# Performance work log

Measured on AMD Instinct MI355X. Metric: run time of the kernel, lower is better.

The kernel has to match this reference:

```python
import jax, jax.numpy as jnp
import numpy as np

N_NODES = 100000


def sage_conv(x, edge_index, W_l, b_l, W_r):
    # PyG SAGEConv (mean aggr): out = lin_l(mean_{j in N(i)} x_j) + lin_r(x_i)
    src, dst = edge_index[0], edge_index[1]
    msgs = x[src]                                  # [E, F] gather
    agg = jax.ops.segment_sum(msgs, dst, num_segments=N_NODES)  # [N, F]
    deg = jax.ops.segment_sum(jnp.ones_like(src, dtype=x.dtype), dst, num_segments=N_NODES)
    mean = agg / jnp.maximum(deg, 1.0)[:, None]
    return mean @ W_l.T + b_l + x @ W_r.T


def setup_inputs() -> dict:
    key = jax.random.key(0)
    ks = jax.random.split(key, 12)
    D_in, D_h, D_e = 128, 256, 64
    E = 1600000
    x = jax.random.normal(ks[0], (N_NODES, D_in), dtype=jnp.float32)
    edge_index = jax.random.randint(ks[1], (2, E), 0, N_NODES, dtype=jnp.int64)

    def lin(k, out_d, in_d):
        s = 1.0 / np.sqrt(in_d)
        return jax.random.uniform(k, (out_d, in_d), jnp.float32, -s, s)

    params = {
        'W_l1': lin(ks[2], D_h, D_in), 'b_l1': jnp.zeros((D_h,), jnp.float32),
        'W_r1': lin(ks[3], D_h, D_in),
        'W_l2': lin(ks[4], D_e, D_h), 'b_l2': jnp.zeros((D_e,), jnp.float32),
        'W_r2': lin(ks[5], D_e, D_h),
        'fc1_W': lin(ks[6], D_h, D_e), 'fc1_b': jnp.zeros((D_h,), jnp.float32),
        'fc2_W': lin(ks[7], D_in, D_h), 'fc2_b': jnp.zeros((D_in,), jnp.float32),
    }
    return {'x': x, 'edge_index': edge_index, **params}


def reference(x, edge_index, W_l1, b_l1, W_r1, W_l2, b_l2, W_r2, fc1_W, fc1_b, fc2_W, fc2_b):
    # Encoder: two SAGEConv layers on LineItem nodes
    h = jax.nn.relu(sage_conv(x, edge_index, W_l1, b_l1, W_r1))
    emb = sage_conv(h, edge_index, W_l2, b_l2, W_r2)
    # Decoder: 2-layer MLP
    hid = jax.nn.relu(emb @ fc1_W.T + fc1_b)
    recon = hid @ fc2_W.T + fc2_b
    return emb, recon
```

## Files before the change

kernel.cpp:

```cpp
#include <hip/hip_runtime.h>
#include <hip/hip_bf16.h>

#define N_NODES 100000
#define D_IN 128
#define D_H 256
#define D_E 64
#define MT 32
#define BSHIFT 9
#define NBUCK ((N_NODES + 511) >> BSHIFT)
#define CHUNK 8192
#define RCR_T 1024
#define RCR_ILP (CHUNK / RCR_T)

typedef __attribute__((ext_vector_type(8))) short short8;
typedef __attribute__((ext_vector_type(4))) float floatx4;

__device__ inline unsigned short f2bf(float f) {
    union { float f; unsigned u; } v; v.f = f;
    unsigned r = v.u + 0x7FFF + ((v.u >> 16) & 1);
    return (unsigned short)(r >> 16);
}
__device__ inline unsigned f2bf2(float a, float b) {
    return (unsigned)f2bf(a) | ((unsigned)f2bf(b) << 16);
}
__device__ inline float2 bf2f2(unsigned v) {
    union { unsigned u; float f; } lo, hi;
    lo.u = v << 16;
    hi.u = v & 0xffff0000u;
    return make_float2(lo.f, hi.f);
}

#define MFMA16(a, b, c) __builtin_amdgcn_mfma_f32_16x16x32_bf16((a), (b), (c), 0, 0, 0)

__global__ void convert_weights(const float* __restrict__ Wl1, const float* __restrict__ Wr1,
                                const float* __restrict__ Wl2, const float* __restrict__ Wr2,
                                const float* __restrict__ fc1W, const float* __restrict__ fc2W,
                                unsigned short* __restrict__ W1s, unsigned short* __restrict__ W2s,
                                unsigned short* __restrict__ F1s, unsigned short* __restrict__ F2s) {
    int idx = blockIdx.x * blockDim.x + threadIdx.x;
    if (idx < 65536) {
        int out = idx >> 8, k = idx & 255;
        float v = (k < 128) ? Wl1[out * 128 + k] : Wr1[out * 128 + (k - 128)];
        int ks = k >> 5, quad = (k >> 3) & 3, e = k & 7, col = out & 15;
        int g = (out >> 4) * 8 + ks;
        W1s[(g * 64 + quad * 16 + col) * 8 + e] = f2bf(v);
    } else if (idx < 98304) {
        int i = idx - 65536; int out = i >> 8, k = i & 255;
        float v = (out < 64) ? Wl2[out * 256 + k] : Wr2[(out - 64) * 256 + k];
        int ks = k >> 5, quad = (k >> 3) & 3, e = k & 7, col = out & 15;
        int g = (out >> 4) * 8 + ks;
        W2s[(g * 64 + quad * 16 + col) * 8 + e] = f2bf(v);
    } else if (idx < 114688) {
        int i = idx - 98304;
        int out = i >> 6, k = i & 63;
        float v = fc1W[i];
        int ks = k >> 5, quad = (k >> 3) & 3, e = k & 7, col = out & 15;
        int g = (out >> 4) * 2 + ks;
        F1s[(g * 64 + quad * 16 + col) * 8 + e] = f2bf(v);
    } else if (idx < 147456) {
        int i = idx - 114688;
        int out = i >> 8, k = i & 255;
        float v = fc2W[i];
        int ks = k >> 5, quad = (k >> 3) & 3, e = k & 7, col = out & 15;
        int g = (out >> 4) * 8 + ks;
        F2s[(g * 64 + quad * 16 + col) * 8 + e] = f2bf(v);
    }
}

__global__ void convert_x(const float4* __restrict__ x4, uint2* __restrict__ xbf2, int total4) {
    int idx = blockIdx.x * blockDim.x + threadIdx.x;
    if (idx >= total4) return;
    float4 v = x4[idx];
    uint2 o;
    o.x = f2bf2(v.x, v.y);
    o.y = f2bf2(v.z, v.w);
    xbf2[idx] = o;
}

__global__ __launch_bounds__(RCR_T) void bucket_hist(
        const int* __restrict__ dst, int* __restrict__ bucketCnt, int E) {
    __shared__ int hist[256];
    const int t = threadIdx.x;
    if (t < 256) hist[t] = 0;
    __syncthreads();
    const int e0 = blockIdx.x * CHUNK;
    if (e0 + CHUNK <= E) {
        int dv[RCR_ILP];
#pragma unroll
        for (int i = 0; i < RCR_ILP; i++) dv[i] = dst[e0 + t + i * RCR_T];
#pragma unroll
        for (int i = 0; i < RCR_ILP; i++) atomicAdd(&hist[dv[i] >> BSHIFT], 1);
    } else {
        for (int e = e0 + t; e < E; e += RCR_T)
            atomicAdd(&hist[dst[e] >> BSHIFT], 1);
    }
    __syncthreads();
    if (t < NBUCK && hist[t] > 0) atomicAdd(&bucketCnt[t * 16], hist[t]);
}

__global__ void bucket_scan(const int* __restrict__ bucketCnt,
                            int* __restrict__ bucketOffs) {
    __shared__ int s[256];
    int t = threadIdx.x;
    int v = (t < NBUCK) ? bucketCnt[t * 16] : 0;
    s[t] = v;
    __syncthreads();
    for (int off = 1; off < 256; off <<= 1) {
        int tv = (t >= off) ? s[t - off] : 0;
        __syncthreads();
        s[t] += tv;
        __syncthreads();
    }
    if (t < NBUCK) bucketOffs[t] = s[t] - v;
    if (t == NBUCK - 1) bucketOffs[NBUCK] = s[t];
}

__global__ __launch_bounds__(RCR_T) void radix_count_reserve(
        const int* __restrict__ src, const int* __restrict__ dst,
        const int* __restrict__ bucketOffs, int* __restrict__ gcur,
        unsigned* __restrict__ pairs, int E) {
    __shared__ int hist[256];
    __shared__ int sBase[256];
    __shared__ int sCur[256];
    const int t = threadIdx.x;
    if (t < 256) { hist[t] = 0; sCur[t] = 0; }
    __syncthreads();
    const int e0 = blockIdx.x * CHUNK;

    if (e0 + CHUNK <= E) {
        int dv[RCR_ILP], sv[RCR_ILP];
#pragma unroll
        for (int i = 0; i < RCR_ILP; i++) dv[i] = dst[e0 + t + i * RCR_T];
#pragma unroll
        for (int i = 0; i < RCR_ILP; i++) atomicAdd(&hist[dv[i] >> BSHIFT], 1);
        __syncthreads();
        if (t < NBUCK && hist[t] > 0)
            sBase[t] = bucketOffs[t] + atomicAdd(&gcur[t * 16], hist[t]);
        __syncthreads();
#pragma unroll
        for (int i = 0; i < RCR_ILP; i++) sv[i] = src[e0 + t + i * RCR_T];
#pragma unroll
        for (int i = 0; i < RCR_ILP; i++) {
            int d = dv[i];
            int b = d >> BSHIFT;
            int pos = sBase[b] + atomicAdd(&sCur[b], 1);
            pairs[pos] = (unsigned)sv[i] | ((unsigned)(d & 511) << 20);
        }
    } else {
        const int e1 = E;
        for (int e = e0 + t; e < e1; e += RCR_T)
            atomicAdd(&hist[dst[e] >> BSHIFT], 1);
        __syncthreads();
        if (t < NBUCK && hist[t] > 0)
            sBase[t] = bucketOffs[t] + atomicAdd(&gcur[t * 16], hist[t]);
        __syncthreads();
        for (int e = e0 + t; e < e1; e += RCR_T) {
            int d = dst[e];
            int b = d >> BSHIFT;
            int pos = sBase[b] + atomicAdd(&sCur[b], 1);
            pairs[pos] = (unsigned)src[e] | ((unsigned)(d & 511) << 20);
        }
    }
}

__global__ __launch_bounds__(512) void radix_scatter2(
        const unsigned* __restrict__ pairs, const int* __restrict__ bucketOffs,
        int* __restrict__ degI, int* __restrict__ offs,
        int* __restrict__ srcS) {
    __shared__ int sCnt[512];
    __shared__ int sOff[512];
    const int b = blockIdx.x;
    const int lo = b << BSHIFT;
    const int t = threadIdx.x;
    sCnt[t] = 0;
    __syncthreads();
    const int start = bucketOffs[b];
    const int end = bucketOffs[b + 1];
    for (int i = start + t; i < end; i += 512)
        atomicAdd(&sCnt[pairs[i] >> 20], 1);
    __syncthreads();
    int v = sCnt[t];
    sOff[t] = v;
    __syncthreads();
    for (int off = 1; off < 512; off <<= 1) {
        int tv = (t >= off) ? sOff[t - off] : 0;
        __syncthreads();
        sOff[t] += tv;
        __syncthreads();
    }
    int excl = sOff[t] - v;
    int node = lo + t;
    if (node < N_NODES) {
        degI[node] = v;
        offs[node] = start + excl;
    }
    __syncthreads();
    sCnt[t] = start + excl;
    __syncthreads();
    int i = start + t;
    for (; i + 3 * 512 < end; i += 4 * 512) {
        unsigned p0 = pairs[i];
        unsigned p1 = pairs[i + 512];
        unsigned p2 = pairs[i + 1024];
        unsigned p3 = pairs[i + 1536];
        int dl0 = (int)(p0 >> 20), dl1 = (int)(p1 >> 20);
        int dl2 = (int)(p2 >> 20), dl3 = (int)(p3 >> 20);
        int q0 = atomicAdd(&sCnt[dl0], 1);
        int q1 = atomicAdd(&sCnt[dl1], 1);
        int q2 = atomicAdd(&sCnt[dl2], 1);
        int q3 = atomicAdd(&sCnt[dl3], 1);
        srcS[q0] = (int)(p0 & 0xFFFFFu);
        srcS[q1] = (int)(p1 & 0xFFFFFu);
        srcS[q2] = (int)(p2 & 0xFFFFFu);
        srcS[q3] = (int)(p3 & 0xFFFFFu);
    }
    for (; i < end; i += 512) {
        unsigned p = pairs[i];
        int dl = (int)(p >> 20);
        int pos = atomicAdd(&sCnt[dl], 1);
        srcS[pos] = (int)(p & 0xFFFFFu);
    }
}

#define ACC8(v)                                                   \
    { float2 f_;                                                  \
      f_ = bf2f2((v).x); s0 += f_.x; s1 += f_.y;                  \
      f_ = bf2f2((v).y); s2 += f_.x; s3 += f_.y;                  \
      f_ = bf2f2((v).z); s4 += f_.x; s5 += f_.y;                  \
      f_ = bf2f2((v).w); s6 += f_.x; s7 += f_.y; }

__global__ __launch_bounds__(256) void gather_mean_bf(
        const uint4* __restrict__ xb4, const int* __restrict__ srcS,
        const int* __restrict__ offs, const int* __restrict__ degI,
        uint4* __restrict__ mean4) {
    const int wave = threadIdx.x >> 6, lane = threadIdx.x & 63;
    const int q = lane >> 4, l16 = lane & 15;
    const int n = (blockIdx.x * 4 + wave) * 4 + q;
    if (n >= N_NODES) return;
    const int start = offs[n], cnt = degI[n];
    const int* sp = srcS + start;
    float s0 = 0.f, s1 = 0.f, s2 = 0.f, s3 = 0.f;
    float s4 = 0.f, s5 = 0.f, s6 = 0.f, s7 = 0.f;
    int j = 0;
    for (; j + 8 <= cnt; j += 8) {
        int i0 = sp[j],     i1 = sp[j + 1], i2 = sp[j + 2], i3 = sp[j + 3];
        int i4 = sp[j + 4], i5 = sp[j + 5], i6 = sp[j + 6], i7 = sp[j + 7];
        uint4 v0 = xb4[i0 * 16 + l16];
        uint4 v1 = xb4[i1 * 16 + l16];
        uint4 v2 = xb4[i2 * 16 + l16];
        uint4 v3 = xb4[i3 * 16 + l16];
        uint4 v4 = xb4[i4 * 16 + l16];
        uint4 v5 = xb4[i5 * 16 + l16];
        uint4 v6 = xb4[i6 * 16 + l16];
        uint4 v7 = xb4[i7 * 16 + l16];
        ACC8(v0); ACC8(v1); ACC8(v2); ACC8(v3);
        ACC8(v4); ACC8(v5); ACC8(v6); ACC8(v7);
    }
    for (; j + 4 <= cnt; j += 4) {
        int i0 = sp[j], i1 = sp[j + 1], i2 = sp[j + 2], i3 = sp[j + 3];
        uint4 v0 = xb4[i0 * 16 + l16];
        uint4 v1 = xb4[i1 * 16 + l16];
        uint4 v2 = xb4[i2 * 16 + l16];
        uint4 v3 = xb4[i3 * 16 + l16];
        ACC8(v0); ACC8(v1); ACC8(v2); ACC8(v3);
    }
    for (; j < cnt; j++) {
        uint4 v = xb4[sp[j] * 16 + l16];
        ACC8(v);
    }
    float rd = 1.0f / fmaxf((float)cnt, 1.0f);
    uint4 o;
    o.x = f2bf2(s0 * rd, s1 * rd);
    o.y = f2bf2(s2 * rd, s3 * rd);
    o.z = f2bf2(s4 * rd, s5 * rd);
    o.w = f2bf2(s6 * rd, s7 * rd);
    mean4[n * 16 + l16] = o;
}

__global__ __launch_bounds__(256, 4) void layer1_mfma(
        const unsigned* __restrict__ xbfu, const unsigned* __restrict__ meanbf,
        const unsigned short* __restrict__ W1s, const float* __restrict__ bl1,
        const unsigned short* __restrict__ W2s,
        unsigned short* __restrict__ z2bf, float* __restrict__ embOut) {
    __shared__ unsigned short sA[MT][264];
    __shared__ unsigned short sH[MT][264];
    const int tid = threadIdx.x;
    const int node0 = blockIdx.x * MT;

    const uint4* mean4 = (const uint4*)meanbf;
    const uint4* x4    = (const uint4*)xbfu;
#pragma unroll
    for (int it = 0; it < 4; it++) {
        int c = tid + it * 256;
        int row = c >> 5, half = (c >> 4) & 1, ci = c & 15;
        uint4 v = half ? x4[(node0 + row) * 16 + ci]
                       : mean4[(node0 + row) * 16 + ci];
        *(uint4*)&sA[row][half * 128 + ci * 8] = v;
    }
    __syncthreads();

    const int wave = tid >> 6, lane = tid & 63;
    const int col = lane & 15, quad = lane >> 4;

    floatx4 acc[2][4];
    const floatx4 zero = {0.f, 0.f, 0.f, 0.f};
#pragma unroll
    for (int mt = 0; mt < 2; mt++)
#pragma unroll
        for (int nt = 0; nt < 4; nt++) acc[mt][nt] = zero;

    const short8* w1base = (const short8*)W1s + wave * 2048 + lane;
#pragma unroll
    for (int ks = 0; ks < 8; ks++) {
        short8 a0 = *(const short8*)&sA[col][ks * 32 + quad * 8];
        short8 a1 = *(const short8*)&sA[16 + col][ks * 32 + quad * 8];
#pragma unroll
        for (int nt = 0; nt < 4; nt++) {
            short8 b = w1base[(nt * 8 + ks) * 64];
            acc[0][nt] = MFMA16(a0, b, acc[0][nt]);
            acc[1][nt] = MFMA16(a1, b, acc[1][nt]);
        }
    }

#pragma unroll
    for (int nt = 0; nt < 4; nt++) {
        int out = (wave * 4 + nt) * 16 + col;
        float bias = bl1[out];
#pragma unroll
        for (int mt = 0; mt < 2; mt++)
#pragma unroll
            for (int r = 0; r < 4; r++)
                sH[mt * 16 + quad * 4 + r][out] = f2bf(fmaxf(acc[mt][nt][r] + bias, 0.f));
    }
    __syncthreads();

    floatx4 acc2[2][2];
#pragma unroll
    for (int mt = 0; mt < 2; mt++)
#pragma unroll
        for (int nt = 0; nt < 2; nt++) acc2[mt][nt] = zero;

    const short8* w2base = (const short8*)W2s + wave * 1024 + lane;
#pragma unroll
    for (int ks = 0; ks < 8; ks++) {
        short8 h0 = *(const short8*)&sH[col][ks * 32 + quad * 8];
        short8 h1 = *(const short8*)&sH[16 + col][ks * 32 + quad * 8];
#pragma unroll
        for (int nt = 0; nt < 2; nt++) {
            short8 b = w2base[(nt * 8 + ks) * 64];
            acc2[0][nt] = MFMA16(h0, b, acc2[0][nt]);
            acc2[1][nt] = MFMA16(h1, b, acc2[1][nt]);
        }
    }

#pragma unroll
    for (int nt = 0; nt < 2; nt++) {
        int out = (wave * 2 + nt) * 16 + col;
#pragma unroll
        for (int mt = 0; mt < 2; mt++)
#pragma unroll
            for (int r = 0; r < 4; r++) {
                int node = node0 + mt * 16 + quad * 4 + r;
                float v = acc2[mt][nt][r];
                if (out < 64) z2bf[node * 64 + out] = f2bf(v);
                else          embOut[node * 64 + (out - 64)] = v;
            }
    }
}

__global__ __launch_bounds__(256) void gather_emb(
        const uint4* __restrict__ z4, const int* __restrict__ srcS,
        const int* __restrict__ offs, const int* __restrict__ degI,
        const float* __restrict__ bl2, float* __restrict__ emb,
        uint4* __restrict__ emb4) {
    const int wave = threadIdx.x >> 6, lane = threadIdx.x & 63;
    const int g = lane >> 3, l8 = lane & 7;
    const int n = (blockIdx.x * 4 + wave) * 8 + g;
    if (n >= N_NODES) return;
    const int start = offs[n], cnt = degI[n];
    const int* sp = srcS + start;
    float s0 = 0.f, s1 = 0.f, s2 = 0.f, s3 = 0.f;
    float s4 = 0.f, s5 = 0.f, s6 = 0.f, s7 = 0.f;
    int j = 0;
    for (; j + 8 <= cnt; j += 8) {
        int i0 = sp[j],     i1 = sp[j + 1], i2 = sp[j + 2], i3 = sp[j + 3];
        int i4 = sp[j + 4], i5 = sp[j + 5], i6 = sp[j + 6], i7 = sp[j + 7];
        uint4 v0 = z4[i0 * 8 + l8];
        uint4 v1 = z4[i1 * 8 + l8];
        uint4 v2 = z4[i2 * 8 + l8];
        uint4 v3 = z4[i3 * 8 + l8];
        uint4 v4 = z4[i4 * 8 + l8];
        uint4 v5 = z4[i5 * 8 + l8];
        uint4 v6 = z4[i6 * 8 + l8];
        uint4 v7 = z4[i7 * 8 + l8];
        ACC8(v0); ACC8(v1); ACC8(v2); ACC8(v3);
        ACC8(v4); ACC8(v5); ACC8(v6); ACC8(v7);
    }
    for (; j + 4 <= cnt; j += 4) {
        int i0 = sp[j], i1 = sp[j + 1], i2 = sp[j + 2], i3 = sp[j + 3];
        uint4 v0 = z4[i0 * 8 + l8];
        uint4 v1 = z4[i1 * 8 + l8];
        uint4 v2 = z4[i2 * 8 + l8];
        uint4 v3 = z4[i3 * 8 + l8];
        ACC8(v0); ACC8(v1); ACC8(v2); ACC8(v3);
    }
    for (; j < cnt; j++) {
        uint4 v = z4[sp[j] * 8 + l8];
        ACC8(v);
    }
    float rd = 1.0f / fmaxf((float)cnt, 1.0f);
    float4 ra = *(const float4*)&emb[n * 64 + l8 * 8];
    float4 rb = *(const float4*)&emb[n * 64 + l8 * 8 + 4];
    float4 ba = *(const float4*)&bl2[l8 * 8];
    float4 bb = *(const float4*)&bl2[l8 * 8 + 4];
    float e0 = s0 * rd + ba.x + ra.x;
    float e1 = s1 * rd + ba.y + ra.y;
    float e2 = s2 * rd + ba.z + ra.z;
    float e3 = s3 * rd + ba.w + ra.w;
    float e4 = s4 * rd + bb.x + rb.x;
    float e5 = s5 * rd + bb.y + rb.y;
    float e6 = s6 * rd + bb.z + rb.z;
    float e7 = s7 * rd + bb.w + rb.w;
    float4 wa = {e0, e1, e2, e3};
    float4 wb = {e4, e5, e6, e7};
    *(float4*)&emb[n * 64 + l8 * 8] = wa;
    *(float4*)&emb[n * 64 + l8 * 8 + 4] = wb;
    uint4 o;
    o.x = f2bf2(e0, e1);
    o.y = f2bf2(e2, e3);
    o.z = f2bf2(e4, e5);
    o.w = f2bf2(e6, e7);
    emb4[n * 8 + l8] = o;
}

__global__ __launch_bounds__(256, 4) void decoder_mfma(
        const unsigned* __restrict__ embbf,
        const unsigned short* __restrict__ F1s, const float* __restrict__ fc1b,
        const unsigned short* __restrict__ F2s, const float* __restrict__ fc2b,
        float* __restrict__ recon) {
    __shared__ unsigned short sE[MT][72];
    __shared__ unsigned short sH[MT][264];
    const int tid = threadIdx.x;
    const int node0 = blockIdx.x * MT;

    {
        const uint4* e4 = (const uint4*)embbf;
        int row = tid >> 3, ci = tid & 7;
        *(uint4*)&sE[row][ci * 8] = e4[(node0 + row) * 8 + ci];
    }
    __syncthreads();

    const int wave = tid >> 6, lane = tid & 63;
    const int col = lane & 15, quad = lane >> 4;

    floatx4 acc[2][4];
    const floatx4 zero = {0.f, 0.f, 0.f, 0.f};
#pragma unroll
    for (int mt = 0; mt < 2; mt++)
#pragma unroll
        for (int nt = 0; nt < 4; nt++) acc[mt][nt] = zero;

    const short8* f1base = (const short8*)F1s + wave * 512 + lane;
#pragma unroll
    for (int ks = 0; ks < 2; ks++) {
        short8 a0 = *(const short8*)&sE[col][ks * 32 + quad * 8];
        short8 a1 = *(const short8*)&sE[16 + col][ks * 32 + quad * 8];
#pragma unroll
        for (int nt = 0; nt < 4; nt++) {
            short8 b = f1base[(nt * 2 + ks) * 64];
            acc[0][nt] = MFMA16(a0, b, acc[0][nt]);
            acc[1][nt] = MFMA16(a1, b, acc[1][nt]);
        }
    }

#pragma unroll
    for (int nt = 0; nt < 4; nt++) {
        int out = (wave * 4 + nt) * 16 + col;
        float bias = fc1b[out];
#pragma unroll
        for (int mt = 0; mt < 2; mt++)
#pragma unroll
            for (int r = 0; r < 4; r++)
                sH[mt * 16 + quad * 4 + r][out] = f2bf(fmaxf(acc[mt][nt][r] + bias, 0.f));
    }
    __syncthreads();

    floatx4 acc2[2][2];
#pragma unroll
    for (int mt = 0; mt < 2; mt++)
#pragma unroll
        for (int nt = 0; nt < 2; nt++) acc2[mt][nt] = zero;

    const short8* f2base = (const short8*)F2s + wave * 1024 + lane;
#pragma unroll
    for (int ks = 0; ks < 8; ks++) {
        short8 h0 = *(const short8*)&sH[col][ks * 32 + quad * 8];
        short8 h1 = *(const short8*)&sH[16 + col][ks * 32 + quad * 8];
#pragma unroll
        for (int nt = 0; nt < 2; nt++) {
            short8 b = f2base[(nt * 8 + ks) * 64];
            acc2[0][nt] = MFMA16(h0, b, acc2[0][nt]);
            acc2[1][nt] = MFMA16(h1, b, acc2[1][nt]);
        }
    }

#pragma unroll
    for (int nt = 0; nt < 2; nt++) {
        int out = (wave * 2 + nt) * 16 + col;
        float bias = fc2b[out];
#pragma unroll
        for (int mt = 0; mt < 2; mt++)
#pragma unroll
            for (int r = 0; r < 4; r++) {
                int node = node0 + mt * 16 + quad * 4 + r;
                recon[node * 128 + out] = acc2[mt][nt][r] + bias;
            }
    }
}

extern "C" void kernel_launch(void* const* d_in, const int* in_sizes, int n_in,
                              void* d_out, int out_size, void* d_ws, size_t ws_size,
                              hipStream_t stream) {
    const float* x    = (const float*)d_in[0];
    const int*   ei   = (const int*)d_in[1];
    const int E = in_sizes[1] / 2;
    const int* src = ei;
    const int* dst = ei + E;
    const float* Wl1  = (const float*)d_in[2];
    const float* bl1  = (const float*)d_in[3];
    const float* Wr1  = (const float*)d_in[4];
    const float* Wl2  = (const float*)d_in[5];
    const float* bl2  = (const float*)d_in[6];
    const float* Wr2  = (const float*)d_in[7];
    const float* fc1W = (const float*)d_in[8];
    const float* fc1b = (const float*)d_in[9];
    const float* fc2W = (const float*)d_in[10];
    const float* fc2b = (const float*)d_in[11];

    float* out   = (float*)d_out;
    float* emb   = out;
    float* recon = out + (size_t)N_NODES * D_E;

    char* ws = (char*)d_ws;
    unsigned short* xbf    = (unsigned short*)(ws);
    unsigned*       meanbf = (unsigned*)(ws + 25600000);
    unsigned short* z2bf   = (unsigned short*)(ws + 51200000);
    unsigned*       embbf  = (unsigned*)(ws + 64000000);
    int* degI   = (int*)(ws + 76800000);
    int* offs   = (int*)(ws + 77200384);
    int* gcur      = (int*)(ws + 77600768);
    int* bucketCnt = (int*)(ws + 77617152);
    int* bucketOffs= (int*)(ws + 77633536);
    int* srcS   = (int*)(ws + 78001664);
    unsigned short* W1s = (unsigned short*)(ws + 84401664);
    unsigned short* W2s = (unsigned short*)(ws + 84532736);
    unsigned short* F1s = (unsigned short*)(ws + 84598272);
    unsigned short* F2s = (unsigned short*)(ws + 84631040);
    unsigned* pairs = (unsigned*)(ws + 25600000);

    hipMemsetAsync(gcur, 0, 32768, stream);

    convert_weights<<<(147456 + 255) / 256, 256, 0, stream>>>(
        Wl1, Wr1, Wl2, Wr2, fc1W, fc2W, W1s, W2s, F1s, F2s);
    convert_x<<<(N_NODES * 32 + 255) / 256, 256, 0, stream>>>(
        (const float4*)x, (uint2*)xbf, N_NODES * 32);

    const int nChunks = (E + CHUNK - 1) / CHUNK;
    bucket_hist<<<nChunks, RCR_T, 0, stream>>>(dst, bucketCnt, E);
    bucket_scan<<<1, 256, 0, stream>>>(bucketCnt, bucketOffs);
    radix_count_reserve<<<nChunks, RCR_T, 0, stream>>>(
        src, dst, bucketOffs, gcur, pairs, E);
    radix_scatter2<<<NBUCK, 512, 0, stream>>>(
        pairs, bucketOffs, degI, offs, srcS);

    gather_mean_bf<<<(N_NODES + 15) / 16, 256, 0, stream>>>(
        (const uint4*)xbf, srcS, offs, degI, (uint4*)meanbf);
    layer1_mfma<<<N_NODES / MT, 256, 0, stream>>>(
        (const unsigned*)xbf, meanbf, W1s, bl1, W2s, z2bf, emb);

    gather_emb<<<(N_NODES + 31) / 32, 256, 0, stream>>>(
        (const uint4*)z2bf, srcS, offs, degI, bl2, emb, (uint4*)embbf);

    decoder_mfma<<<N_NODES / MT, 256, 0, stream>>>(
        embbf, F1s, fc1b, F2s, fc2b, recon);
}
```

Measured before the change: 324.2 us.

## Fuse neighbor gather-mean into layer1 and decoder MFMA kernels

Merges the layer-1 neighbor mean gather into the layer-1 MFMA kernel, so the bf16 mean rows go straight into shared memory. Likewise merges the layer-2 gather and embedding finalize into the decoder kernel, writing the bf16 embedding tile to shared memory. This removes the meanbf and embbf round trips through global memory and two kernel launches. The cost is that each block now does irregular gather work before its MFMA phase, and the __launch_bounds__(256,4) occupancy limit may reduce the latency hiding available to the gathers.

```diff
diff --git a/kernel.cpp b/kernel.cpp
--- a/kernel.cpp
+++ b/kernel.cpp
@@ -229,56 +229,9 @@
       f_ = bf2f2((v).z); s4 += f_.x; s5 += f_.y;                  \
       f_ = bf2f2((v).w); s6 += f_.x; s7 += f_.y; }
 
-__global__ __launch_bounds__(256) void gather_mean_bf(
+__global__ __launch_bounds__(256, 4) void fused_layer1(
         const uint4* __restrict__ xb4, const int* __restrict__ srcS,
         const int* __restrict__ offs, const int* __restrict__ degI,
-        uint4* __restrict__ mean4) {
-    const int wave = threadIdx.x >> 6, lane = threadIdx.x & 63;
-    const int q = lane >> 4, l16 = lane & 15;
-    const int n = (blockIdx.x * 4 + wave) * 4 + q;
-    if (n >= N_NODES) return;
-    const int start = offs[n], cnt = degI[n];
-    const int* sp = srcS + start;
-    float s0 = 0.f, s1 = 0.f, s2 = 0.f, s3 = 0.f;
-    float s4 = 0.f, s5 = 0.f, s6 = 0.f, s7 = 0.f;
-    int j = 0;
-    for (; j + 8 <= cnt; j += 8) {
-        int i0 = sp[j],     i1 = sp[j + 1], i2 = sp[j + 2], i3 = sp[j + 3];
-        int i4 = sp[j + 4], i5 = sp[j + 5], i6 = sp[j + 6], i7 = sp[j + 7];
-        uint4 v0 = xb4[i0 * 16 + l16];
-        uint4 v1 = xb4[i1 * 16 + l16];
-        uint4 v2 = xb4[i2 * 16 + l16];
-        uint4 v3 = xb4[i3 * 16 + l16];
-        uint4 v4 = xb4[i4 * 16 + l16];
-        uint4 v5 = xb4[i5 * 16 + l16];
-        uint4 v6 = xb4[i6 * 16 + l16];
-        uint4 v7 = xb4[i7 * 16 + l16];
-        ACC8(v0); ACC8(v1); ACC8(v2); ACC8(v3);
-        ACC8(v4); ACC8(v5); ACC8(v6); ACC8(v7);
-    }
-    for (; j + 4 <= cnt; j += 4) {
-        int i0 = sp[j], i1 = sp[j + 1], i2 = sp[j + 2], i3 = sp[j + 3];
-        uint4 v0 = xb4[i0 * 16 + l16];
-        uint4 v1 = xb4[i1 * 16 + l16];
-        uint4 v2 = xb4[i2 * 16 + l16];
-        uint4 v3 = xb4[i3 * 16 + l16];
-        ACC8(v0); ACC8(v1); ACC8(v2); ACC8(v3);
-    }
-    for (; j < cnt; j++) {
-        uint4 v = xb4[sp[j] * 16 + l16];
-        ACC8(v);
-    }
-    float rd = 1.0f / fmaxf((float)cnt, 1.0f);
-    uint4 o;
-    o.x = f2bf2(s0 * rd, s1 * rd);
-    o.y = f2bf2(s2 * rd, s3 * rd);
-    o.z = f2bf2(s4 * rd, s5 * rd);
-    o.w = f2bf2(s6 * rd, s7 * rd);
-    mean4[n * 16 + l16] = o;
-}
-
-__global__ __launch_bounds__(256, 4) void layer1_mfma(
-        const unsigned* __restrict__ xbfu, const unsigned* __restrict__ meanbf,
         const unsigned short* __restrict__ W1s, const float* __restrict__ bl1,
         const unsigned short* __restrict__ W2s,
         unsigned short* __restrict__ z2bf, float* __restrict__ embOut) {
@@ -286,20 +239,62 @@
     __shared__ unsigned short sH[MT][264];
     const int tid = threadIdx.x;
     const int node0 = blockIdx.x * MT;
-
-    const uint4* mean4 = (const uint4*)meanbf;
-    const uint4* x4    = (const uint4*)xbfu;
-#pragma unroll
-    for (int it = 0; it < 4; it++) {
+    const int wave = tid >> 6, lane = tid & 63;
+    const int q = lane >> 4, l16 = lane & 15;
+
+#pragma unroll
+    for (int it = 0; it < 2; it++) {
         int c = tid + it * 256;
-        int row = c >> 5, half = (c >> 4) & 1, ci = c & 15;
-        uint4 v = half ? x4[(node0 + row) * 16 + ci]
-                       : mean4[(node0 + row) * 16 + ci];
-        *(uint4*)&sA[row][half * 128 + ci * 8] = v;
-    }
-    __syncthreads();
-
-    const int wave = tid >> 6, lane = tid & 63;
+        int row = c >> 4, ci = c & 15;
+        *(uint4*)&sA[row][128 + ci * 8] = xb4[(node0 + row) * 16 + ci];
+    }
+
+    const int qid = wave * 4 + q;
+#pragma unroll
+    for (int half = 0; half < 2; half++) {
+        const int nl = qid * 2 + half;
+        const int n = node0 + nl;
+        const int start = offs[n], cnt = degI[n];
+        const int* sp = srcS + start;
+        float s0 = 0.f, s1 = 0.f, s2 = 0.f, s3 = 0.f;
+        float s4 = 0.f, s5 = 0.f, s6 = 0.f, s7 = 0.f;
+        int j = 0;
+        for (; j + 8 <= cnt; j += 8) {
+            int i0 = sp[j],     i1 = sp[j + 1], i2 = sp[j + 2], i3 = sp[j + 3];
+            int i4 = sp[j + 4], i5 = sp[j + 5], i6 = sp[j + 6], i7 = sp[j + 7];
+            uint4 v0 = xb4[i0 * 16 + l16];
+            uint4 v1 = xb4[i1 * 16 + l16];
+            uint4 v2 = xb4[i2 * 16 + l16];
+            uint4 v3 = xb4[i3 * 16 + l16];
+            uint4 v4 = xb4[i4 * 16 + l16];
+            uint4 v5 = xb4[i5 * 16 + l16];
+            uint4 v6 = xb4[i6 * 16 + l16];
+            uint4 v7 = xb4[i7 * 16 + l16];
+            ACC8(v0); ACC8(v1); ACC8(v2); ACC8(v3);
+            ACC8(v4); ACC8(v5); ACC8(v6); ACC8(v7);
+        }
+        for (; j + 4 <= cnt; j += 4) {
+            int i0 = sp[j], i1 = sp[j + 1], i2 = sp[j + 2], i3 = sp[j + 3];
+            uint4 v0 = xb4[i0 * 16 + l16];
+            uint4 v1 = xb4[i1 * 16 + l16];
+            uint4 v2 = xb4[i2 * 16 + l16];
+            uint4 v3 = xb4[i3 * 16 + l16];
+            ACC8(v0); ACC8(v1); ACC8(v2); ACC8(v3);
+        }
+        for (; j < cnt; j++) {
+            uint4 v = xb4[sp[j] * 16 + l16];
+            ACC8(v);
+        }
+        float rd = 1.0f / fmaxf((float)cnt, 1.0f);
+        uint4 o;
+        o.x = f2bf2(s0 * rd, s1 * rd);
+        o.y = f2bf2(s2 * rd, s3 * rd);
+        o.z = f2bf2(s4 * rd, s5 * rd);
+        o.w = f2bf2(s6 * rd, s7 * rd);
+        *(uint4*)&sA[nl][l16 * 8] = o;
+    }
+    __syncthreads();
+
     const int col = lane & 15, quad = lane >> 4;
 
     floatx4 acc[2][4];
@@ -368,73 +363,10 @@
     }
 }
 
-__global__ __launch_bounds__(256) void gather_emb(
+__global__ __launch_bounds__(256, 4) void fused_decoder(
         const uint4* __restrict__ z4, const int* __restrict__ srcS,
         const int* __restrict__ offs, const int* __restrict__ degI,
         const float* __restrict__ bl2, float* __restrict__ emb,
-        uint4* __restrict__ emb4) {
-    const int wave = threadIdx.x >> 6, lane = threadIdx.x & 63;
-    const int g = lane >> 3, l8 = lane & 7;
-    const int n = (blockIdx.x * 4 + wave) * 8 + g;
-    if (n >= N_NODES) return;
-    const int start = offs[n], cnt = degI[n];
-    const int* sp = srcS + start;
-    float s0 = 0.f, s1 = 0.f, s2 = 0.f, s3 = 0.f;
-    float s4 = 0.f, s5 = 0.f, s6 = 0.f, s7 = 0.f;
-    int j = 0;
-    for (; j + 8 <= cnt; j += 8) {
-        int i0 = sp[j],     i1 = sp[j + 1], i2 = sp[j + 2], i3 = sp[j + 3];
-        int i4 = sp[j + 4], i5 = sp[j + 5], i6 = sp[j + 6], i7 = sp[j + 7];
-        uint4 v0 = z4[i0 * 8 + l8];
-        uint4 v1 = z4[i1 * 8 + l8];
-        uint4 v2 = z4[i2 * 8 + l8];
-        uint4 v3 = z4[i3 * 8 + l8];
-        uint4 v4 = z4[i4 * 8 + l8];
-        uint4 v5 = z4[i5 * 8 + l8];
-        uint4 v6 = z4[i6 * 8 + l8];
-        uint4 v7 = z4[i7 * 8 + l8];
-        ACC8(v0); ACC8(v1); ACC8(v2); ACC8(v3);
-        ACC8(v4); ACC8(v5); ACC8(v6); ACC8(v7);
-    }
-    for (; j + 4 <= cnt; j += 4) {
-        int i0 = sp[j], i1 = sp[j + 1], i2 = sp[j + 2], i3 = sp[j + 3];
-        uint4 v0 = z4[i0 * 8 + l8];
-        uint4 v1 = z4[i1 * 8 + l8];
-        uint4 v2 = z4[i2 * 8 + l8];
-        uint4 v3 = z4[i3 * 8 + l8];
-        ACC8(v0); ACC8(v1); ACC8(v2); ACC8(v3);
-    }
-    for (; j < cnt; j++) {
-        uint4 v = z4[sp[j] * 8 + l8];
-        ACC8(v);
-    }
-    float rd = 1.0f / fmaxf((float)cnt, 1.0f);
-    float4 ra = *(const float4*)&emb[n * 64 + l8 * 8];
-    float4 rb = *(const float4*)&emb[n * 64 + l8 * 8 + 4];
-    float4 ba = *(const float4*)&bl2[l8 * 8];
-    float4 bb = *(const float4*)&bl2[l8 * 8 + 4];
-    float e0 = s0 * rd + ba.x + ra.x;
-    float e1 = s1 * rd + ba.y + ra.y;
-    float e2 = s2 * rd + ba.z + ra.z;
-    float e3 = s3 * rd + ba.w + ra.w;
-    float e4 = s4 * rd + bb.x + rb.x;
-    float e5 = s5 * rd + bb.y + rb.y;
-    float e6 = s6 * rd + bb.z + rb.z;
-    float e7 = s7 * rd + bb.w + rb.w;
-    float4 wa = {e0, e1, e2, e3};
-    float4 wb = {e4, e5, e6, e7};
-    *(float4*)&emb[n * 64 + l8 * 8] = wa;
-    *(float4*)&emb[n * 64 + l8 * 8 + 4] = wb;
-    uint4 o;
-    o.x = f2bf2(e0, e1);
-    o.y = f2bf2(e2, e3);
-    o.z = f2bf2(e4, e5);
-    o.w = f2bf2(e6, e7);
-    emb4[n * 8 + l8] = o;
-}
-
-__global__ __launch_bounds__(256, 4) void decoder_mfma(
-        const unsigned* __restrict__ embbf,
         const unsigned short* __restrict__ F1s, const float* __restrict__ fc1b,
         const unsigned short* __restrict__ F2s, const float* __restrict__ fc2b,
         float* __restrict__ recon) {
@@ -442,15 +374,69 @@
     __shared__ unsigned short sH[MT][264];
     const int tid = threadIdx.x;
     const int node0 = blockIdx.x * MT;
+    const int wave = tid >> 6, lane = tid & 63;
+    const int g = lane >> 3, l8 = lane & 7;
 
     {
-        const uint4* e4 = (const uint4*)embbf;
-        int row = tid >> 3, ci = tid & 7;
-        *(uint4*)&sE[row][ci * 8] = e4[(node0 + row) * 8 + ci];
-    }
-    __syncthreads();
-
-    const int wave = tid >> 6, lane = tid & 63;
+        const int nl = wave * 8 + g;
+        const int n = node0 + nl;
+        const int start = offs[n], cnt = degI[n];
+        const int* sp = srcS + start;
+        float s0 = 0.f, s1 = 0.f, s2 = 0.f, s3 = 0.f;
+        float s4 = 0.f, s5 = 0.f, s6 = 0.f, s7 = 0.f;
+        int j = 0;
+        for (; j + 8 <= cnt; j += 8) {
+            int i0 = sp[j],     i1 = sp[j + 1], i2 = sp[j + 2], i3 = sp[j + 3];
+            int i4 = sp[j + 4], i5 = sp[j + 5], i6 = sp[j + 6], i7 = sp[j + 7];
+            uint4 v0 = z4[i0 * 8 + l8];
+            uint4 v1 = z4[i1 * 8 + l8];
+            uint4 v2 = z4[i2 * 8 + l8];
+            uint4 v3 = z4[i3 * 8 + l8];
+            uint4 v4 = z4[i4 * 8 + l8];
+            uint4 v5 = z4[i5 * 8 + l8];
+            uint4 v6 = z4[i6 * 8 + l8];
+            uint4 v7 = z4[i7 * 8 + l8];
+            ACC8(v0); ACC8(v1); ACC8(v2); ACC8(v3);
+            ACC8(v4); ACC8(v5); ACC8(v6); ACC8(v7);
+        }
+        for (; j + 4 <= cnt; j += 4) {
+            int i0 = sp[j], i1 = sp[j + 1], i2 = sp[j + 2], i3 = sp[j + 3];
+            uint4 v0 = z4[i0 * 8 + l8];
+            uint4 v1 = z4[i1 * 8 + l8];
+            uint4 v2 = z4[i2 * 8 + l8];
+            uint4 v3 = z4[i3 * 8 + l8];
+            ACC8(v0); ACC8(v1); ACC8(v2); ACC8(v3);
+        }
+        for (; j < cnt; j++) {
+            uint4 v = z4[sp[j] * 8 + l8];
+            ACC8(v);
+        }
+        float rd = 1.0f / fmaxf((float)cnt, 1.0f);
+        float4 ra = *(const float4*)&emb[n * 64 + l8 * 8];
+        float4 rb = *(const float4*)&emb[n * 64 + l8 * 8 + 4];
+        float4 ba = *(const float4*)&bl2[l8 * 8];
+        float4 bb = *(const float4*)&bl2[l8 * 8 + 4];
+        float e0 = s0 * rd + ba.x + ra.x;
+        float e1 = s1 * rd + ba.y + ra.y;
+        float e2 = s2 * rd + ba.z + ra.z;
+        float e3 = s3 * rd + ba.w + ra.w;
+        float e4 = s4 * rd + bb.x + rb.x;
+        float e5 = s5 * rd + bb.y + rb.y;
+        float e6 = s6 * rd + bb.z + rb.z;
+        float e7 = s7 * rd + bb.w + rb.w;
+        float4 wa = {e0, e1, e2, e3};
+        float4 wb = {e4, e5, e6, e7};
+        *(float4*)&emb[n * 64 + l8 * 8] = wa;
+        *(float4*)&emb[n * 64 + l8 * 8 + 4] = wb;
+        uint4 o;
+        o.x = f2bf2(e0, e1);
+        o.y = f2bf2(e2, e3);
+        o.z = f2bf2(e4, e5);
+        o.w = f2bf2(e6, e7);
+        *(uint4*)&sE[nl][l8 * 8] = o;
+    }
+    __syncthreads();
+
     const int col = lane & 15, quad = lane >> 4;
 
     floatx4 acc[2][4];
@@ -543,9 +529,7 @@
 
     char* ws = (char*)d_ws;
     unsigned short* xbf    = (unsigned short*)(ws);
-    unsigned*       meanbf = (unsigned*)(ws + 25600000);
     unsigned short* z2bf   = (unsigned short*)(ws + 51200000);
-    unsigned*       embbf  = (unsigned*)(ws + 64000000);
     int* degI   = (int*)(ws + 76800000);
     int* offs   = (int*)(ws + 77200384);
     int* gcur      = (int*)(ws + 77600768);
@@ -573,14 +557,10 @@
     radix_scatter2<<<NBUCK, 512, 0, stream>>>(
         pairs, bucketOffs, degI, offs, srcS);
 
-    gather_mean_bf<<<(N_NODES + 15) / 16, 256, 0, stream>>>(
-        (const uint4*)xbf, srcS, offs, degI, (uint4*)meanbf);
-    layer1_mfma<<<N_NODES / MT, 256, 0, stream>>>(
-        (const unsigned*)xbf, meanbf, W1s, bl1, W2s, z2bf, emb);
-
-    gather_emb<<<(N_NODES + 31) / 32, 256, 0, stream>>>(
-        (const uint4*)z2bf, srcS, offs, degI, bl2, emb, (uint4*)embbf);
-
-    decoder_mfma<<<N_NODES / MT, 256, 0, stream>>>(
-        embbf, F1s, fc1b, F2s, fc2b, recon);
-}
+    fused_layer1<<<N_NODES / MT, 256, 0, stream>>>(
+        (const uint4*)xbf, srcS, offs, degI, W1s, bl1, W2s, z2bf, emb);
+
+    fused_decoder<<<N_NODES / MT, 256, 0, stream>>>(
+        (const uint4*)z2bf, srcS, offs, degI, bl2, emb,
+        F1s, fc1b, F2s, fc2b, recon);
+}
```

Result: faster. 315.5 us (-2.7%).
